# Performance work log

Measured on AMD Instinct MI355X. Metric: run time of the kernel, lower is better.

## Reference

```python
import jax, jax.numpy as jnp
import numpy as np

B, T, N = 1024, 256, 64  # batch, seq_len, n_labels


def setup_inputs() -> dict:
    key = jax.random.key(0)
    k1, k2, k3, k4, k5 = jax.random.split(key, 5)
    emit = jax.random.normal(k1, (B, T, N), dtype=jnp.float32)
    lens = jax.random.randint(k2, (B,), T // 2, T + 1)
    mask = jnp.arange(T)[None, :] < lens[:, None]  # [B, T] bool, monotone
    trans = 0.1 * jax.random.normal(k3, (N, N), dtype=jnp.float32)
    strans = 0.1 * jax.random.normal(k4, (N,), dtype=jnp.float32)
    etrans = 0.1 * jax.random.normal(k5, (N,), dtype=jnp.float32)
    return {"emit": emit, "trans": trans, "strans": strans,
            "etrans": etrans, "mask": mask}


def reference(emit, trans, strans, etrans, mask):
    """CRF partition function (Tagger.get_logZ), summed over the batch."""
    lse = jax.scipy.special.logsumexp
    # row-normalize transitions in log space (as in the torch module)
    strans_n = strans - lse(strans)
    etrans_n = etrans - lse(etrans)
    trans_n = trans - lse(trans, axis=-1, keepdims=True)  # [N, N]

    e = jnp.transpose(emit, (1, 0, 2))  # [T, B, N]
    m = mask.T                          # [T, B]

    alpha0 = strans_n + e[0]            # [B, N]

    def step(alpha, xs):
        emit_t, mask_t = xs             # [B, N], [B]
        # scores[b, k] = logsumexp_j(alpha[b, j] + trans[j, k] + emit_t[b, k])
        scores = lse(alpha[:, :, None] + trans_n[None, :, :]
                     + emit_t[:, None, :], axis=1)
        alpha = jnp.where(mask_t[:, None], scores, alpha)
        return alpha, None

    alpha, _ = jax.lax.scan(step, alpha0, (e[1:], m[1:]))
    logZ = jnp.sum(lse(alpha + etrans_n, axis=1))
    return logZ
```

## Files before the change

### kernel.cpp

```cpp
#include <hip/hip_runtime.h>


#define CRF_B 1024
#define CRF_T 256
#define CRF_N 64

__device__ __forceinline__ float rl0(float x) {
    return __int_as_float(__builtin_amdgcn_readfirstlane(__float_as_int(x)));
}
__device__ __forceinline__ float rlane(float x, int j) {
    return __int_as_float(__builtin_amdgcn_readlane(__float_as_int(x), j));
}

__device__ __forceinline__ float wave_lse(float v) {
    float m = v;
    #pragma unroll
    for (int off = 1; off < 64; off <<= 1) m = fmaxf(m, __shfl_xor(m, off));
    float s = __expf(v - m);
    #pragma unroll
    for (int off = 1; off < 64; off <<= 1) s += __shfl_xor(s, off);
    return m + __logf(s);
}

__launch_bounds__(256, 1)
__attribute__((amdgpu_waves_per_eu(1, 1)))
__global__ void crf_fwd_kernel(const float* __restrict__ emit,
                               const float* __restrict__ trans,
                               const float* __restrict__ strans,
                               const float* __restrict__ etrans,
                               const unsigned char* __restrict__ mask_u8,
                               float* __restrict__ out)
{
    const int tid  = threadIdx.x;
    const int lane = tid & 63;
    const int wid  = tid >> 6;
    const int b    = blockIdx.x * 4 + wid;

    float rowlse_v;
    {
        const float* rowp = trans + lane * CRF_N;
        float m = -1e30f;
        #pragma unroll 8
        for (int k = 0; k < CRF_N; ++k) m = fmaxf(m, rowp[k]);
        float s = 0.f;
        #pragma unroll 8
        for (int k = 0; k < CRF_N; ++k) s += __expf(rowp[k] - m);
        rowlse_v = m + __logf(s);
    }

    float Ecol[CRF_N];
    #pragma unroll
    for (int j = 0; j < CRF_N; ++j)
        Ecol[j] = trans[j * CRF_N + lane] - rlane(rowlse_v, j);
    float cmx = -1e30f;
    #pragma unroll
    for (int j = 0; j < CRF_N; ++j) cmx = fmaxf(cmx, Ecol[j]);
    #pragma unroll
    for (int j = 0; j < CRF_N; ++j) Ecol[j] = __expf(Ecol[j] - cmx);

    const float sn = wave_lse(strans[lane]);

    int len;
    {
        int c8 = 0;
        #pragma unroll
        for (int q = 0; q < 4; ++q)
            c8 += (mask_u8[(size_t)b * CRF_T + q * 64 + lane] != 0) ? 1 : 0;
        for (int off = 1; off < 64; off <<= 1) c8 += __shfl_xor(c8, off);
        if (c8 >= 128) {
            len = c8;
        } else {
            const int* mi = (const int*)mask_u8;
            int ci = 0;
            #pragma unroll
            for (int q = 0; q < 4; ++q)
                ci += (mi[(size_t)b * CRF_T + q * 64 + lane] != 0) ? 1 : 0;
            for (int off = 1; off < 64; off <<= 1) ci += __shfl_xor(ci, off);
            len = ci;
        }
    }

    const float* eb = emit + (size_t)b * CRF_T * CRF_N;

    float alpha0 = (strans[lane] - sn) + eb[lane];
    float c0 = rl0(alpha0);
    float u  = __expf(alpha0 - c0);
    float R  = 1.0f;
    float Pm = 1.0f;
    int   Eacc = 0;
    const float c0_keep = c0;

#define CRF_STEP(EE)                                                     \
    {                                                                    \
        float s0 = 0.f, s1 = 0.f, s2 = 0.f, s3 = 0.f;                    \
        _Pragma("unroll")                                                \
        for (int g = 0; g < 4; ++g) {                                    \
            float w[16];                                                 \
            _Pragma("unroll")                                            \
            for (int i = 0; i < 16; ++i) w[i] = rlane(u, 16 * g + i);    \
            _Pragma("unroll")                                            \
            for (int i = 0; i < 16; i += 4) {                            \
                s0 = fmaf(w[i + 0], Ecol[16 * g + i + 0], s0);           \
                s1 = fmaf(w[i + 1], Ecol[16 * g + i + 1], s1);           \
                s2 = fmaf(w[i + 2], Ecol[16 * g + i + 2], s2);           \
                s3 = fmaf(w[i + 3], Ecol[16 * g + i + 3], s3);           \
            }                                                            \
        }                                                                \
        float s = (s0 + s1) + (s2 + s3);                                 \
        u = s * (R * (EE));                                              \
        float u0 = rl0(u);                                               \
        R = __builtin_amdgcn_rcpf(u0);                                   \
        Pm *= u0;                                                        \
    }

    float eN[4], eeC[4];
    #pragma unroll
    for (int d = 0; d < 4; ++d) eN[d] = eb[(size_t)(1 + d) * CRF_N + lane];
    #pragma unroll
    for (int d = 0; d < 4; ++d) eeC[d] = __expf(eN[d] + cmx);

    int t0 = 1;
    while (t0 + 4 <= len) {
        #pragma unroll
        for (int d = 0; d < 4; ++d) {
            int ti = t0 + 4 + d;
            ti = (ti < len) ? ti : (len - 1);
            eN[d] = eb[(size_t)ti * CRF_N + lane];
        }
        CRF_STEP(eeC[0]); CRF_STEP(eeC[1]);
        CRF_STEP(eeC[2]); CRF_STEP(eeC[3]);
        {
            int ex;
            Pm = frexpf(Pm, &ex);
            Eacc += ex;
        }
        #pragma unroll
        for (int d = 0; d < 4; ++d) eeC[d] = __expf(eN[d] + cmx);
        t0 += 4;
    }
    {
        const int nrem = len - t0;
        #pragma unroll
        for (int d = 0; d < 4; ++d) {
            if (d >= nrem) break;
            CRF_STEP(eeC[d]);
        }
    }
#undef CRF_STEP

    const float en = wave_lse(etrans[lane]);
    float Lacc = c0_keep + 0.6931471805599453f * (float)Eacc + __logf(Pm);
    float v = Lacc + __logf(u * R) + (etrans[lane] - en);
    float m = v;
    #pragma unroll
    for (int off = 1; off < 64; off <<= 1) m = fmaxf(m, __shfl_xor(m, off));
    float sum = __expf(v - m);
    #pragma unroll
    for (int off = 1; off < 64; off <<= 1) sum += __shfl_xor(sum, off);

    if (lane == 0) {
        atomicAdd(out, m + __logf(sum));
    }
}

extern "C" void kernel_launch(void* const* d_in, const int* in_sizes, int n_in,
                              void* d_out, int out_size, void* d_ws, size_t ws_size,
                              hipStream_t stream) {
    const float* emit   = (const float*)d_in[0];
    const float* trans  = (const float*)d_in[1];
    const float* strans = (const float*)d_in[2];
    const float* etrans = (const float*)d_in[3];
    const unsigned char* mask = (const unsigned char*)d_in[4];
    float* out = (float*)d_out;

    hipMemsetAsync(out, 0, sizeof(float), stream);
    crf_fwd_kernel<<<dim3(CRF_B / 4), dim3(256), 0, stream>>>(
        emit, trans, strans, etrans, mask, out);
}
```

Baseline: 158.0 us.

## Use bf16 dot2 for CRF recurrence with packed transitions and one wave per block

The exp-transition column is stored as 32 packed bf16 pairs instead of 64 fp32 registers. Each step packs alpha pairs through a DPP swap and perm, then accumulates with v_dot2_f32_bf16, which halves the readlane and FMA count on the serial critical path. The normaliser now comes from a readfirstlane of the raw sum times a precomputed lane-0 emission scalar, which takes the readfirstlane of u off the dependency chain. The launch changes to one 64-thread block per sequence without the waves_per_eu constraint. The cost is reduced precision in alpha and the transitions, accumulated over up to 255 steps.

Measured after the change: 142.6 us. 9.7% less time.

```diff
diff --git a/kernel.cpp b/kernel.cpp
--- a/kernel.cpp
+++ b/kernel.cpp
@@ -5,10 +5,12 @@
 #define CRF_T 256
 #define CRF_N 64
 
+typedef __bf16 bf16x2 __attribute__((ext_vector_type(2)));
+
 __device__ __forceinline__ float rl0(float x) {
     return __int_as_float(__builtin_amdgcn_readfirstlane(__float_as_int(x)));
 }
-__device__ __forceinline__ float rlane(float x, int j) {
+__device__ __forceinline__ float rlanef(float x, int j) {
     return __int_as_float(__builtin_amdgcn_readlane(__float_as_int(x), j));
 }
 
@@ -22,8 +24,31 @@
     return m + __logf(s);
 }
 
-__launch_bounds__(256, 1)
-__attribute__((amdgpu_waves_per_eu(1, 1)))
+__device__ __forceinline__ unsigned bf16_rne(float f) {
+    unsigned u = __float_as_uint(f);
+    return (u + 0x7FFFu + ((u >> 16) & 1u)) >> 16;
+}
+
+__device__ __forceinline__ unsigned pack_pairs(float u) {
+    unsigned pa = __float_as_uint(u) + 0x8000u;
+    unsigned pb = (unsigned)__builtin_amdgcn_update_dpp(
+        0, (int)pa, 0xB1 , 0xF, 0xF, false);
+    return __builtin_amdgcn_perm(pb, pa, 0x07060302);
+}
+
+__device__ __forceinline__ float dot2bf(unsigned a, unsigned b, float c) {
+#if __has_builtin(__builtin_amdgcn_fdot2_f32_bf16)
+    return __builtin_amdgcn_fdot2_f32_bf16(__builtin_bit_cast(bf16x2, a),
+                                           __builtin_bit_cast(bf16x2, b),
+                                           c, false);
+#else
+    float d = c;
+    asm("v_dot2_f32_bf16 %0, %1, %2, %0" : "+v"(d) : "v"(a), "v"(b));
+    return d;
+#endif
+}
+
+__launch_bounds__(64, 1)
 __global__ void crf_fwd_kernel(const float* __restrict__ emit,
                                const float* __restrict__ trans,
                                const float* __restrict__ strans,
@@ -31,10 +56,8 @@
                                const unsigned char* __restrict__ mask_u8,
                                float* __restrict__ out)
 {
-    const int tid  = threadIdx.x;
-    const int lane = tid & 63;
-    const int wid  = tid >> 6;
-    const int b    = blockIdx.x * 4 + wid;
+    const int lane = threadIdx.x;
+    const int b    = blockIdx.x;
 
     float rowlse_v;
     {
@@ -48,15 +71,18 @@
         rowlse_v = m + __logf(s);
     }
 
-    float Ecol[CRF_N];
+    float cmx = -1e30f;
     #pragma unroll
     for (int j = 0; j < CRF_N; ++j)
-        Ecol[j] = trans[j * CRF_N + lane] - rlane(rowlse_v, j);
-    float cmx = -1e30f;
-    #pragma unroll
-    for (int j = 0; j < CRF_N; ++j) cmx = fmaxf(cmx, Ecol[j]);
-    #pragma unroll
-    for (int j = 0; j < CRF_N; ++j) Ecol[j] = __expf(Ecol[j] - cmx);
+        cmx = fmaxf(cmx, trans[j * CRF_N + lane] - rlanef(rowlse_v, j));
+
+    unsigned Epk[32];
+    #pragma unroll
+    for (int m = 0; m < 32; ++m) {
+        float e0 = __expf(trans[(2 * m)     * CRF_N + lane] - rlanef(rowlse_v, 2 * m)     - cmx);
+        float e1 = __expf(trans[(2 * m + 1) * CRF_N + lane] - rlanef(rowlse_v, 2 * m + 1) - cmx);
+        Epk[m] = bf16_rne(e0) | (bf16_rne(e1) << 16);
+    }
 
     const float sn = wave_lse(strans[lane]);
 
@@ -85,39 +111,43 @@
     float alpha0 = (strans[lane] - sn) + eb[lane];
     float c0 = rl0(alpha0);
     float u  = __expf(alpha0 - c0);
+    unsigned upi = pack_pairs(u);
     float R  = 1.0f;
     float Pm = 1.0f;
     int   Eacc = 0;
-    const float c0_keep = c0;
-
-#define CRF_STEP(EE)                                                     \
-    {                                                                    \
-        float s0 = 0.f, s1 = 0.f, s2 = 0.f, s3 = 0.f;                    \
-        _Pragma("unroll")                                                \
-        for (int g = 0; g < 4; ++g) {                                    \
-            float w[16];                                                 \
-            _Pragma("unroll")                                            \
-            for (int i = 0; i < 16; ++i) w[i] = rlane(u, 16 * g + i);    \
-            _Pragma("unroll")                                            \
-            for (int i = 0; i < 16; i += 4) {                            \
-                s0 = fmaf(w[i + 0], Ecol[16 * g + i + 0], s0);           \
-                s1 = fmaf(w[i + 1], Ecol[16 * g + i + 1], s1);           \
-                s2 = fmaf(w[i + 2], Ecol[16 * g + i + 2], s2);           \
-                s3 = fmaf(w[i + 3], Ecol[16 * g + i + 3], s3);           \
-            }                                                            \
-        }                                                                \
-        float s = (s0 + s1) + (s2 + s3);                                 \
-        u = s * (R * (EE));                                              \
-        float u0 = rl0(u);                                               \
-        R = __builtin_amdgcn_rcpf(u0);                                   \
-        Pm *= u0;                                                        \
-    }
-
-    float eN[4], eeC[4];
+
+#define CRF_STEP(EE, EE0)                                                   \
+    {                                                                       \
+        float ree = R * (EE);               \
+        float sc0 = R * (EE0);                                              \
+        float a0 = 0.f, a1 = 0.f, a2 = 0.f, a3 = 0.f;                       \
+        _Pragma("unroll")                                                   \
+        for (int m2 = 0; m2 < 32; m2 += 4) {                                \
+            unsigned w0 = (unsigned)__builtin_amdgcn_readlane((int)upi, 2 * m2 + 0); \
+            unsigned w1 = (unsigned)__builtin_amdgcn_readlane((int)upi, 2 * m2 + 2); \
+            unsigned w2 = (unsigned)__builtin_amdgcn_readlane((int)upi, 2 * m2 + 4); \
+            unsigned w3 = (unsigned)__builtin_amdgcn_readlane((int)upi, 2 * m2 + 6); \
+            a0 = dot2bf(w0, Epk[m2 + 0], a0);                               \
+            a1 = dot2bf(w1, Epk[m2 + 1], a1);                               \
+            a2 = dot2bf(w2, Epk[m2 + 2], a2);                               \
+            a3 = dot2bf(w3, Epk[m2 + 3], a3);                               \
+        }                                                                   \
+        float s = (a0 + a1) + (a2 + a3);                                    \
+        float s0 = rl0(s);                                                  \
+        u = s * ree;                                                        \
+        upi = pack_pairs(u);                                                \
+        float u0 = s0 * sc0;              \
+        R = __builtin_amdgcn_rcpf(u0);                                      \
+        Pm *= u0;                                                           \
+    }
+
+    float eN[4], eeC[4], ee0C[4];
     #pragma unroll
     for (int d = 0; d < 4; ++d) eN[d] = eb[(size_t)(1 + d) * CRF_N + lane];
     #pragma unroll
     for (int d = 0; d < 4; ++d) eeC[d] = __expf(eN[d] + cmx);
+    #pragma unroll
+    for (int d = 0; d < 4; ++d) ee0C[d] = rl0(eeC[d]);
 
     int t0 = 1;
     while (t0 + 4 <= len) {
@@ -127,8 +157,8 @@
             ti = (ti < len) ? ti : (len - 1);
             eN[d] = eb[(size_t)ti * CRF_N + lane];
         }
-        CRF_STEP(eeC[0]); CRF_STEP(eeC[1]);
-        CRF_STEP(eeC[2]); CRF_STEP(eeC[3]);
+        CRF_STEP(eeC[0], ee0C[0]); CRF_STEP(eeC[1], ee0C[1]);
+        CRF_STEP(eeC[2], ee0C[2]); CRF_STEP(eeC[3], ee0C[3]);
         {
             int ex;
             Pm = frexpf(Pm, &ex);
@@ -136,6 +166,8 @@
         }
         #pragma unroll
         for (int d = 0; d < 4; ++d) eeC[d] = __expf(eN[d] + cmx);
+        #pragma unroll
+        for (int d = 0; d < 4; ++d) ee0C[d] = rl0(eeC[d]);
         t0 += 4;
     }
     {
@@ -143,13 +175,13 @@
         #pragma unroll
         for (int d = 0; d < 4; ++d) {
             if (d >= nrem) break;
-            CRF_STEP(eeC[d]);
+            CRF_STEP(eeC[d], ee0C[d]);
         }
     }
 #undef CRF_STEP
 
     const float en = wave_lse(etrans[lane]);
-    float Lacc = c0_keep + 0.6931471805599453f * (float)Eacc + __logf(Pm);
+    float Lacc = c0 + 0.6931471805599453f * (float)Eacc + __logf(Pm);
     float v = Lacc + __logf(u * R) + (etrans[lane] - en);
     float m = v;
     #pragma unroll
@@ -174,6 +206,6 @@
     float* out = (float*)d_out;
 
     hipMemsetAsync(out, 0, sizeof(float), stream);
-    crf_fwd_kernel<<<dim3(CRF_B / 4), dim3(256), 0, stream>>>(
+    crf_fwd_kernel<<<dim3(CRF_B), dim3(64), 0, stream>>>(
         emit, trans, strans, etrans, mask, out);
 }
```

## Replace per-step readlane matvec with bf16 MFMA using runtime-probed lane layout

Applied to the files above, without the earlier changes.

Each recurrence step's 64x64 matrix-vector product, previously 64 readlanes plus 64 FMAs per lane, now runs as eight 16x16x32 bf16 MFMAs. The alpha vector is republished through LDS and packed to bf16 every step. The MFMA output-lane and operand-row mapping is found at runtime with probe MFMAs, and an atomicMin picks one writer lane per column. The launch changes from 4 waves per block to one wave per block, one batch row each. This targets the serial per-step latency, but bf16 weights and state lose precision and each step now carries an LDS round trip.

New measurement: 183.1 us. 1.16x slower.

```diff
diff --git a/kernel.cpp b/kernel.cpp
--- a/kernel.cpp
+++ b/kernel.cpp
@@ -5,13 +5,22 @@
 #define CRF_T 256
 #define CRF_N 64
 
+typedef short s16x8 __attribute__((ext_vector_type(8)));
+typedef float f32x4 __attribute__((ext_vector_type(4)));
+typedef int   i32x4 __attribute__((ext_vector_type(4)));
+
+#define MFMA_BF16 __builtin_amdgcn_mfma_f32_16x16x32_bf16
+
 __device__ __forceinline__ float rl0(float x) {
     return __int_as_float(__builtin_amdgcn_readfirstlane(__float_as_int(x)));
 }
-__device__ __forceinline__ float rlane(float x, int j) {
+__device__ __forceinline__ float rlanef(float x, int j) {
     return __int_as_float(__builtin_amdgcn_readlane(__float_as_int(x), j));
 }
-
+__device__ __forceinline__ float bperm_f(float v, int srclane) {
+    return __int_as_float(
+        __builtin_amdgcn_ds_bpermute(srclane << 2, __float_as_int(v)));
+}
 __device__ __forceinline__ float wave_lse(float v) {
     float m = v;
     #pragma unroll
@@ -22,7 +31,20 @@
     return m + __logf(s);
 }
 
-__launch_bounds__(256, 1)
+__device__ __forceinline__ unsigned bf16_rne(float f) {
+    unsigned u = __float_as_uint(f);
+    return (u + 0x7FFFu + ((u >> 16) & 1u)) >> 16;
+}
+__device__ __forceinline__ unsigned bfb(float f) {
+    return __float_as_uint(f) >> 16;
+}
+__device__ __forceinline__ int pk2(float x, float y) {
+    unsigned ax = __float_as_uint(x) + 0x8000u;
+    unsigned ay = __float_as_uint(y) + 0x8000u;
+    return (int)__builtin_amdgcn_perm(ay, ax, 0x07060302);
+}
+
+__launch_bounds__(64, 1)
 __attribute__((amdgpu_waves_per_eu(1, 1)))
 __global__ void crf_fwd_kernel(const float* __restrict__ emit,
                                const float* __restrict__ trans,
@@ -31,10 +53,14 @@
                                const unsigned char* __restrict__ mask_u8,
                                float* __restrict__ out)
 {
-    const int tid  = threadIdx.x;
-    const int lane = tid & 63;
-    const int wid  = tid >> 6;
-    const int b    = blockIdx.x * 4 + wid;
+    const int lane  = threadIdx.x;
+    const int b     = blockIdx.x;
+    const int c     = lane & 15;
+    const int q     = lane >> 4;
+    const int rstar = lane & 3;
+
+    __shared__ __align__(16) float    u_f[CRF_N];
+    __shared__ unsigned owner16[16];
 
     float rowlse_v;
     {
@@ -48,15 +74,81 @@
         rowlse_v = m + __logf(s);
     }
 
-    float Ecol[CRF_N];
-    #pragma unroll
-    for (int j = 0; j < CRF_N; ++j)
-        Ecol[j] = trans[j * CRF_N + lane] - rlane(rowlse_v, j);
-    float cmx = -1e30f;
-    #pragma unroll
-    for (int j = 0; j < CRF_N; ++j) cmx = fmaxf(cmx, Ecol[j]);
-    #pragma unroll
-    for (int j = 0; j < CRF_N; ++j) Ecol[j] = __expf(Ecol[j] - cmx);
+    const f32x4 zz = {0.f, 0.f, 0.f, 0.f};
+
+    int cm;
+    {
+        unsigned one_b = bfb(1.0f);
+        i32x4 av = {(int)(one_b | (one_b << 16)), (int)(one_b | (one_b << 16)),
+                    (int)(one_b | (one_b << 16)), (int)(one_b | (one_b << 16))};
+        unsigned cb = bfb((float)c);
+        i32x4 bv = {(int)(cb | (cb << 16)), (int)(cb | (cb << 16)),
+                    (int)(cb | (cb << 16)), (int)(cb | (cb << 16))};
+        f32x4 pr = MFMA_BF16(__builtin_bit_cast(s16x8, av),
+                             __builtin_bit_cast(s16x8, bv), zz, 0, 0, 0);
+        float v = pr[rstar] * 0.03125f;
+        cm = ((int)(v + 0.5f)) & 15;
+    }
+
+    int rpi[8];
+    {
+        i32x4 aenc;
+        #pragma unroll
+        for (int p = 0; p < 4; ++p)
+            aenc[p] = (int)(bfb((float)(8 * q + 2 * p)) |
+                            (bfb((float)(8 * q + 2 * p + 1)) << 16));
+        s16x8 Aenc = __builtin_bit_cast(s16x8, aenc);
+        float p32   = (float)(1 << (5 * q));
+        float p32in = __builtin_amdgcn_rcpf(p32);
+        unsigned wb = bfb(p32);
+        #pragma unroll
+        for (int j0 = 0; j0 < 8; ++j0) {
+            i32x4 bv = {0, 0, 0, 0};
+            bv[j0 >> 1] = (j0 & 1) ? (int)(wb << 16) : (int)wb;
+            f32x4 pr = MFMA_BF16(Aenc, __builtin_bit_cast(s16x8, bv),
+                                 zz, 0, 0, 0);
+            float t = floorf(pr[0] * p32in);
+            rpi[j0] = ((int)t) & 31;
+        }
+    }
+
+    if (lane < 16) owner16[lane] = 64u;
+    __builtin_amdgcn_wave_barrier();
+    atomicMin(&owner16[cm], (unsigned)lane);
+    __builtin_amdgcn_wave_barrier();
+    const bool iswr = (owner16[cm] == (unsigned)lane);
+
+    float cmxB[4], cmxW[4];
+    #pragma unroll
+    for (int n = 0; n < 4; ++n) { cmxB[n] = -1e30f; cmxW[n] = -1e30f; }
+    for (int j = 0; j < CRF_N; ++j) {
+        float rl = rlanef(rowlse_v, j);
+        #pragma unroll
+        for (int n = 0; n < 4; ++n) {
+            cmxB[n] = fmaxf(cmxB[n], trans[j * CRF_N + 16 * n + c]  - rl);
+            cmxW[n] = fmaxf(cmxW[n], trans[j * CRF_N + 16 * n + cm] - rl);
+        }
+    }
+
+    s16x8 Bf[2][4];
+    #pragma unroll
+    for (int h = 0; h < 2; ++h) {
+        #pragma unroll
+        for (int n = 0; n < 4; ++n) {
+            i32x4 acc;
+            #pragma unroll
+            for (int p = 0; p < 4; ++p) {
+                int r0 = 32 * h + rpi[2 * p];
+                int r1 = 32 * h + rpi[2 * p + 1];
+                float rls0 = bperm_f(rowlse_v, r0);
+                float rls1 = bperm_f(rowlse_v, r1);
+                float e0 = __expf(trans[r0 * CRF_N + 16 * n + c] - rls0 - cmxB[n]);
+                float e1 = __expf(trans[r1 * CRF_N + 16 * n + c] - rls1 - cmxB[n]);
+                acc[p] = (int)(bf16_rne(e0) | (bf16_rne(e1) << 16));
+            }
+            Bf[h][n] = __builtin_bit_cast(s16x8, acc);
+        }
+    }
 
     const float sn = wave_lse(strans[lane]);
 
@@ -64,8 +156,8 @@
     {
         int c8 = 0;
         #pragma unroll
-        for (int q = 0; q < 4; ++q)
-            c8 += (mask_u8[(size_t)b * CRF_T + q * 64 + lane] != 0) ? 1 : 0;
+        for (int qq = 0; qq < 4; ++qq)
+            c8 += (mask_u8[(size_t)b * CRF_T + qq * 64 + lane] != 0) ? 1 : 0;
         for (int off = 1; off < 64; off <<= 1) c8 += __shfl_xor(c8, off);
         if (c8 >= 128) {
             len = c8;
@@ -73,8 +165,8 @@
             const int* mi = (const int*)mask_u8;
             int ci = 0;
             #pragma unroll
-            for (int q = 0; q < 4; ++q)
-                ci += (mi[(size_t)b * CRF_T + q * 64 + lane] != 0) ? 1 : 0;
+            for (int qq = 0; qq < 4; ++qq)
+                ci += (mi[(size_t)b * CRF_T + qq * 64 + lane] != 0) ? 1 : 0;
             for (int off = 1; off < 64; off <<= 1) ci += __shfl_xor(ci, off);
             len = ci;
         }
@@ -82,42 +174,81 @@
 
     const float* eb = emit + (size_t)b * CRF_T * CRF_N;
 
-    float alpha0 = (strans[lane] - sn) + eb[lane];
-    float c0 = rl0(alpha0);
-    float u  = __expf(alpha0 - c0);
-    float R  = 1.0f;
-    float Pm = 1.0f;
-    int   Eacc = 0;
-    const float c0_keep = c0;
-
-#define CRF_STEP(EE)                                                     \
-    {                                                                    \
-        float s0 = 0.f, s1 = 0.f, s2 = 0.f, s3 = 0.f;                    \
-        _Pragma("unroll")                                                \
-        for (int g = 0; g < 4; ++g) {                                    \
-            float w[16];                                                 \
-            _Pragma("unroll")                                            \
-            for (int i = 0; i < 16; ++i) w[i] = rlane(u, 16 * g + i);    \
-            _Pragma("unroll")                                            \
-            for (int i = 0; i < 16; i += 4) {                            \
-                s0 = fmaf(w[i + 0], Ecol[16 * g + i + 0], s0);           \
-                s1 = fmaf(w[i + 1], Ecol[16 * g + i + 1], s1);           \
-                s2 = fmaf(w[i + 2], Ecol[16 * g + i + 2], s2);           \
-                s3 = fmaf(w[i + 3], Ecol[16 * g + i + 3], s3);           \
-            }                                                            \
-        }                                                                \
-        float s = (s0 + s1) + (s2 + s3);                                 \
-        u = s * (R * (EE));                                              \
-        float u0 = rl0(u);                                               \
-        R = __builtin_amdgcn_rcpf(u0);                                   \
-        Pm *= u0;                                                        \
-    }
-
-    float eN[4], eeC[4];
-    #pragma unroll
-    for (int d = 0; d < 4; ++d) eN[d] = eb[(size_t)(1 + d) * CRF_N + lane];
-    #pragma unroll
-    for (int d = 0; d < 4; ++d) eeC[d] = __expf(eN[d] + cmx);
+    float un[4];
+    float R = 1.0f, Pm = 1.0f;
+    int Eacc = 0;
+    float c0;
+    {
+        float a0[4];
+        #pragma unroll
+        for (int n = 0; n < 4; ++n)
+            a0[n] = (strans[16 * n + cm] - sn) + eb[16 * n + cm];
+        c0 = rl0(a0[0]);
+        #pragma unroll
+        for (int n = 0; n < 4; ++n) un[n] = __expf(a0[n] - c0);
+    }
+
+    s16x8 A0f, A1f;
+
+#define PUB_LOAD()                                                           \
+    {                                                                        \
+        if (iswr) {                                                          \
+            u_f[cm]      = un[0];                                            \
+            u_f[16 + cm] = un[1];                                            \
+            u_f[32 + cm] = un[2];                                            \
+            u_f[48 + cm] = un[3];                                            \
+        }                                                                    \
+        __builtin_amdgcn_wave_barrier();                                     \
+        f32x4 va = *(const f32x4*)&u_f[8 * q];                               \
+        f32x4 vb = *(const f32x4*)&u_f[8 * q + 4];                           \
+        f32x4 vc = *(const f32x4*)&u_f[32 + 8 * q];                          \
+        f32x4 vd = *(const f32x4*)&u_f[32 + 8 * q + 4];                      \
+        i32x4 wa = {pk2(va[0], va[1]), pk2(va[2], va[3]),                    \
+                    pk2(vb[0], vb[1]), pk2(vb[2], vb[3])};                   \
+        i32x4 wbv = {pk2(vc[0], vc[1]), pk2(vc[2], vc[3]),                   \
+                     pk2(vd[0], vd[1]), pk2(vd[2], vd[3])};                  \
+        A0f = __builtin_bit_cast(s16x8, wa);                                 \
+        A1f = __builtin_bit_cast(s16x8, wbv);                                \
+        __builtin_amdgcn_wave_barrier();                                     \
+    }
+
+    PUB_LOAD();
+
+#define CRF_STEP(EE)                                                         \
+    {                                                                        \
+        float Ree0 = R * (EE)[0];                                            \
+        float Ree1 = R * (EE)[1];                                            \
+        float Ree2 = R * (EE)[2];                                            \
+        float Ree3 = R * (EE)[3];                                            \
+        f32x4 p0 = MFMA_BF16(A0f, Bf[0][0], zz, 0, 0, 0);                    \
+        f32x4 p1 = MFMA_BF16(A0f, Bf[0][1], zz, 0, 0, 0);                    \
+        f32x4 p2 = MFMA_BF16(A0f, Bf[0][2], zz, 0, 0, 0);                    \
+        f32x4 p3 = MFMA_BF16(A0f, Bf[0][3], zz, 0, 0, 0);                    \
+        f32x4 q0 = MFMA_BF16(A1f, Bf[1][0], p0, 0, 0, 0);                    \
+        f32x4 q1 = MFMA_BF16(A1f, Bf[1][1], p1, 0, 0, 0);                    \
+        f32x4 q2 = MFMA_BF16(A1f, Bf[1][2], p2, 0, 0, 0);                    \
+        f32x4 q3 = MFMA_BF16(A1f, Bf[1][3], p3, 0, 0, 0);                    \
+        un[0] = q0[rstar] * Ree0;                                            \
+        un[1] = q1[rstar] * Ree1;                                            \
+        un[2] = q2[rstar] * Ree2;                                            \
+        un[3] = q3[rstar] * Ree3;                                            \
+        float u0 = rl0(un[0]);                                               \
+        R = __builtin_amdgcn_rcpf(u0);                                       \
+        Pm *= u0;                                                            \
+        PUB_LOAD();                                                          \
+    }
+
+    float eN[4][4], eeC[4][4];
+    #pragma unroll
+    for (int d = 0; d < 4; ++d)
+        #pragma unroll
+        for (int n = 0; n < 4; ++n)
+            eN[d][n] = eb[(size_t)(1 + d) * CRF_N + 16 * n + cm];
+    #pragma unroll
+    for (int d = 0; d < 4; ++d)
+        #pragma unroll
+        for (int n = 0; n < 4; ++n)
+            eeC[d][n] = __expf(eN[d][n] + cmxW[n]);
 
     int t0 = 1;
     while (t0 + 4 <= len) {
@@ -125,7 +256,9 @@
         for (int d = 0; d < 4; ++d) {
             int ti = t0 + 4 + d;
             ti = (ti < len) ? ti : (len - 1);
-            eN[d] = eb[(size_t)ti * CRF_N + lane];
+            #pragma unroll
+            for (int n = 0; n < 4; ++n)
+                eN[d][n] = eb[(size_t)ti * CRF_N + 16 * n + cm];
         }
         CRF_STEP(eeC[0]); CRF_STEP(eeC[1]);
         CRF_STEP(eeC[2]); CRF_STEP(eeC[3]);
@@ -135,7 +268,10 @@
             Eacc += ex;
         }
         #pragma unroll
-        for (int d = 0; d < 4; ++d) eeC[d] = __expf(eN[d] + cmx);
+        for (int d = 0; d < 4; ++d)
+            #pragma unroll
+            for (int n = 0; n < 4; ++n)
+                eeC[d][n] = __expf(eN[d][n] + cmxW[n]);
         t0 += 4;
     }
     {
@@ -147,14 +283,26 @@
         }
     }
 #undef CRF_STEP
+#undef PUB_LOAD
 
     const float en = wave_lse(etrans[lane]);
-    float Lacc = c0_keep + 0.6931471805599453f * (float)Eacc + __logf(Pm);
-    float v = Lacc + __logf(u * R) + (etrans[lane] - en);
-    float m = v;
+    float Lacc = c0 + 0.6931471805599453f * (float)Eacc + __logf(Pm);
+    float vm = -1e30f;
+    float v4[4];
+    #pragma unroll
+    for (int n = 0; n < 4; ++n) {
+        v4[n] = Lacc + __logf(un[n] * R) + (etrans[16 * n + cm] - en);
+        vm = fmaxf(vm, v4[n]);
+    }
+    float vs = 0.f;
+    #pragma unroll
+    for (int n = 0; n < 4; ++n) vs += __expf(v4[n] - vm);
+    float Lf = iswr ? (vm + __logf(vs)) : -1e30f;
+
+    float m = Lf;
     #pragma unroll
     for (int off = 1; off < 64; off <<= 1) m = fmaxf(m, __shfl_xor(m, off));
-    float sum = __expf(v - m);
+    float sum = __expf(Lf - m);
     #pragma unroll
     for (int off = 1; off < 64; off <<= 1) sum += __shfl_xor(sum, off);
 
@@ -174,6 +322,6 @@
     float* out = (float*)d_out;
 
     hipMemsetAsync(out, 0, sizeof(float), stream);
-    crf_fwd_kernel<<<dim3(CRF_B / 4), dim3(256), 0, stream>>>(
+    crf_fwd_kernel<<<dim3(CRF_B), dim3(64), 0, stream>>>(
         emit, trans, strans, etrans, mask, out);
 }
```
